# Performance work log

Measured on AMD Instinct MI355X. Metric: run time of the kernel, lower is better.

The kernel has to match this reference:

```python
import jax, jax.numpy as jnp
import numpy as np

TEMPERATURE = 8.0  # sqrt(d_k)
WINDOW = 2
GATE_THRESH = 0.5
NEG_INF = -1e30


def setup_inputs() -> dict:
    key = jax.random.key(0)
    k1, k2, k3, k4 = jax.random.split(key, 4)
    BH, L, D = 32, 2048, 64
    return {
        "q": jax.random.normal(k1, (BH, L, D), dtype=jnp.float32),
        "k": jax.random.normal(k2, (BH, L, D), dtype=jnp.float32),
        "v": jax.random.normal(k3, (BH, L, D), dtype=jnp.float32),
        "gate_w": jax.random.normal(k4, (1, D), dtype=jnp.float32) * 0.1,
        "gate_b": jnp.zeros((1,), dtype=jnp.float32),
    }


def reference(q, k, v, gate_w, gate_b):
    # q,k: [BH, L, D]; v: [BH, L, Dv]
    BH, Lq, D = q.shape
    Lk = k.shape[1]
    attn = jnp.einsum("bqd,bkd->bqk", q, k) / TEMPERATURE  # [BH, Lq, Lk]
    # per-query gate: if sigmoid(linear(q)) <= thresh, restrict to sliding window
    gate = jax.nn.sigmoid(jnp.einsum("bqd,od->bqo", q, gate_w) + gate_b) > GATE_THRESH  # [BH,Lq,1]
    i = jnp.arange(Lq)[:, None]
    j = jnp.arange(Lk)[None, :]
    window_ok = jnp.abs(i - j) <= WINDOW  # [Lq, Lk]; equals left=max(0,i-W), right=min(Lk,i+W+1)
    allowed = gate | window_ok[None, :, :]  # gate True -> full attention
    attn = jnp.where(allowed, attn, NEG_INF)
    attn = jax.nn.softmax(attn, axis=2)
    # dropout omitted (eval mode)
    out = jnp.einsum("bqk,bkd->bqd", attn, v)
    return out, attn
```

## Files before the change

kernel.cpp:

```cpp
#include <hip/hip_runtime.h>


typedef short bf16x8 __attribute__((ext_vector_type(8)));
typedef float f32x4  __attribute__((ext_vector_type(4)));

#define LSEQ 2048
#define DDIM 64
#define PB_STRIDE 36
#define OS_STRIDE 68

__device__ __forceinline__ unsigned short f2bf(float x) {
    unsigned int u = __float_as_uint(x);
    u += 0x7FFFu + ((u >> 16) & 1u);
    return (unsigned short)(u >> 16);
}

__device__ __forceinline__ unsigned int pk2f(float a, float b) {
    return (unsigned int)f2bf(a) | ((unsigned int)f2bf(b) << 16);
}

__device__ __forceinline__ unsigned int pk2u(unsigned short a, unsigned short b) {
    return (unsigned int)a | ((unsigned int)b << 16);
}

__device__ __forceinline__ float pick5(int jj, float e0, float e1, float e2,
                                       float e3, float e4) {
    float r = 0.f;
    r = (jj == 0) ? e0 : r;
    r = (jj == 1) ? e1 : r;
    r = (jj == 2) ? e2 : r;
    r = (jj == 3) ? e3 : r;
    r = (jj == 4) ? e4 : r;
    return r;
}

__global__ __launch_bounds__(256)
void dsa_prep(const float* __restrict__ K, const float* __restrict__ V,
              unsigned short* __restrict__ Kb, unsigned short* __restrict__ Vt)
{
    const int bh  = blockIdx.x >> 5;
    const int k0  = (blockIdx.x & 31) << 6;
    const int tid = threadIdx.x;
    __shared__ unsigned short tileT[64][73];

    const int key = tid >> 2;
    const int d0  = (tid & 3) << 4;
    const float* srcK = K + ((size_t)bh * LSEQ + k0 + key) * DDIM + d0;
    const float* srcV = V + ((size_t)bh * LSEQ + k0 + key) * DDIM + d0;
    {
        uint4 w0, w1;
        w0.x = pk2f(srcK[0],  srcK[1]);  w0.y = pk2f(srcK[2],  srcK[3]);
        w0.z = pk2f(srcK[4],  srcK[5]);  w0.w = pk2f(srcK[6],  srcK[7]);
        w1.x = pk2f(srcK[8],  srcK[9]);  w1.y = pk2f(srcK[10], srcK[11]);
        w1.z = pk2f(srcK[12], srcK[13]); w1.w = pk2f(srcK[14], srcK[15]);
        unsigned short* dst = Kb + ((size_t)bh * LSEQ + k0 + key) * DDIM + d0;
        *(uint4*)(dst)     = w0;
        *(uint4*)(dst + 8) = w1;
    }
    #pragma unroll
    for (int j = 0; j < 16; ++j) tileT[d0 + j][key] = f2bf(srcV[j]);
    __syncthreads();
    {
        const int d   = tid >> 2;
        const int kk0 = (tid & 3) << 4;
        uint4 w0, w1;
        w0.x = pk2u(tileT[d][kk0 + 0],  tileT[d][kk0 + 1]);
        w0.y = pk2u(tileT[d][kk0 + 2],  tileT[d][kk0 + 3]);
        w0.z = pk2u(tileT[d][kk0 + 4],  tileT[d][kk0 + 5]);
        w0.w = pk2u(tileT[d][kk0 + 6],  tileT[d][kk0 + 7]);
        w1.x = pk2u(tileT[d][kk0 + 8],  tileT[d][kk0 + 9]);
        w1.y = pk2u(tileT[d][kk0 + 10], tileT[d][kk0 + 11]);
        w1.z = pk2u(tileT[d][kk0 + 12], tileT[d][kk0 + 13]);
        w1.w = pk2u(tileT[d][kk0 + 14], tileT[d][kk0 + 15]);
        unsigned short* dst = Vt + (size_t)bh * DDIM * LSEQ + (size_t)d * LSEQ + k0 + kk0;
        *(uint4*)(dst)     = w0;
        *(uint4*)(dst + 8) = w1;
    }
}

__global__ __launch_bounds__(256)
void dsa_main(const float* __restrict__ Q,
              const unsigned short* __restrict__ Kb,
              const unsigned short* __restrict__ Vt,
              const float* __restrict__ K32,
              const float* __restrict__ V32,
              const float* __restrict__ GW,
              const float* __restrict__ GB,
              float* __restrict__ OUT,
              float* __restrict__ ATT)
{
    __shared__ float Pbuf[4][2][16 * PB_STRIDE];
    __shared__ float dsum[4][16];
    __shared__ float osum[4][16][OS_STRIDE];
    __shared__ int   sidx[64];
    __shared__ int   gShared;

    const int bx   = blockIdx.x;
    const int bh   = bx >> 5;
    const int q0   = (bx & 31) << 6;
    const int tid  = threadIdx.x;
    const int wave = tid >> 6;
    const int lane = tid & 63;
    const int m16  = lane & 15;
    const int quad = lane >> 4;

    const float* qb = Q + ((size_t)bh * LSEQ + q0) * DDIM;

    if (wave == 0) {
        const float* qr = qb + lane * DDIM;
        float a = 0.f;
        #pragma unroll 8
        for (int d = 0; d < DDIM; ++d) a += qr[d] * GW[d];
        a += GB[0];
        const bool gt = (a > 0.f);
        const unsigned long long b = __ballot(gt);
        const int below = __popcll(b & ((1ull << lane) - 1ull));
        const int gg    = __popcll(b);
        const int pos   = gt ? below : (gg + (lane - below));
        sidx[pos] = lane;
        if (lane == 0) gShared = gg;
    }
    __syncthreads();
    const int g = gShared;
    const int T = (g + 15) >> 4;

    const unsigned short* kbb = Kb + (size_t)bh * LSEQ * DDIM;
    const unsigned short* vtb = Vt + (size_t)bh * DDIM * LSEQ;
    const int kbase = wave << 9;

    for (int t = 0; t < T; ++t) {
        const int  myIdx = (t << 4) + m16;
        const bool valid = myIdx < g;
        const int  srow  = sidx[valid ? myIdx : (g - 1)];

        bf16x8 qfrag[2];
        {
            const float* qr = qb + srow * DDIM + (quad << 3);
            #pragma unroll
            for (int db = 0; db < 2; ++db) {
                const float* p = qr + db * 32;
                bf16x8 f;
                #pragma unroll
                for (int j = 0; j < 8; ++j) f[j] = (short)f2bf(p[j]);
                qfrag[db] = f;
            }
        }

        const unsigned short* kp0 = kbb + (size_t)(kbase + m16) * DDIM + (quad << 3);

        float lsum[4] = {0.f, 0.f, 0.f, 0.f};
        for (int kt = 0; kt < 16; ++kt) {
            const unsigned short* kp = kp0 + (size_t)(kt * 32) * DDIM;
            bf16x8 k0 = *(const bf16x8*)(kp);
            bf16x8 k1 = *(const bf16x8*)(kp + 32);
            bf16x8 k2 = *(const bf16x8*)(kp + 16 * DDIM);
            bf16x8 k3 = *(const bf16x8*)(kp + 16 * DDIM + 32);
            f32x4 a0 = {0.f, 0.f, 0.f, 0.f}, a1 = {0.f, 0.f, 0.f, 0.f};
            a0 = __builtin_amdgcn_mfma_f32_16x16x32_bf16(qfrag[0], k0, a0, 0, 0, 0);
            a0 = __builtin_amdgcn_mfma_f32_16x16x32_bf16(qfrag[1], k1, a0, 0, 0, 0);
            a1 = __builtin_amdgcn_mfma_f32_16x16x32_bf16(qfrag[0], k2, a1, 0, 0, 0);
            a1 = __builtin_amdgcn_mfma_f32_16x16x32_bf16(qfrag[1], k3, a1, 0, 0, 0);
            #pragma unroll
            for (int r = 0; r < 4; ++r)
                lsum[r] += __expf(a0[r] * 0.125f) + __expf(a1[r] * 0.125f);
        }
        #pragma unroll
        for (int r = 0; r < 4; ++r) {
            float x = lsum[r];
            x += __shfl_xor(x, 1); x += __shfl_xor(x, 2);
            x += __shfl_xor(x, 4); x += __shfl_xor(x, 8);
            if (m16 == 0) dsum[wave][(quad << 2) + r] = x;
        }
        __syncthreads();

        float inv[4];
        #pragma unroll
        for (int r = 0; r < 4; ++r) {
            const int rr = (quad << 2) + r;
            inv[r] = 1.0f / (dsum[0][rr] + dsum[1][rr] + dsum[2][rr] + dsum[3][rr]);
        }

        f32x4 oacc0 = {0.f,0.f,0.f,0.f}, oacc1 = {0.f,0.f,0.f,0.f};
        f32x4 oacc2 = {0.f,0.f,0.f,0.f}, oacc3 = {0.f,0.f,0.f,0.f};
        float* ap0 = ATT + ((size_t)(bh * LSEQ + q0 + srow)) * LSEQ + kbase + (quad << 3);
        const unsigned short* vp0 = vtb + (size_t)m16 * LSEQ + kbase + (quad << 3);

        #define COMPUTE(KT_) {                                                        \
            const unsigned short* kp = kp0 + (size_t)((KT_) * 32) * DDIM;             \
            bf16x8 k0 = *(const bf16x8*)(kp);                                         \
            bf16x8 k1 = *(const bf16x8*)(kp + 32);                                    \
            bf16x8 k2 = *(const bf16x8*)(kp + 16 * DDIM);                             \
            bf16x8 k3 = *(const bf16x8*)(kp + 16 * DDIM + 32);                        \
            f32x4 a0 = {0.f,0.f,0.f,0.f}, a1 = {0.f,0.f,0.f,0.f};                     \
            a0 = __builtin_amdgcn_mfma_f32_16x16x32_bf16(qfrag[0], k0, a0, 0, 0, 0);  \
            a0 = __builtin_amdgcn_mfma_f32_16x16x32_bf16(qfrag[1], k1, a0, 0, 0, 0);  \
            a1 = __builtin_amdgcn_mfma_f32_16x16x32_bf16(qfrag[0], k2, a1, 0, 0, 0);  \
            a1 = __builtin_amdgcn_mfma_f32_16x16x32_bf16(qfrag[1], k3, a1, 0, 0, 0);  \
            float* pw = &Pbuf[wave][(KT_) & 1][0];                                    \
            _Pragma("unroll")                                                         \
            for (int r = 0; r < 4; ++r) {                                             \
                const int prow = (quad << 2) + r;                                     \
                pw[prow * PB_STRIDE + m16]      = __expf(a0[r] * 0.125f) * inv[r];    \
                pw[prow * PB_STRIDE + 16 + m16] = __expf(a1[r] * 0.125f) * inv[r];    \
            }                                                                         \
        }

        #define CONSUME(KT_) {                                                        \
            const float* prd = &Pbuf[wave][(KT_) & 1][0] + m16 * PB_STRIDE + (quad << 3); \
            f32x4 p0 = *(const f32x4*)(prd);                                          \
            f32x4 p1 = *(const f32x4*)(prd + 4);                                      \
            const unsigned short* vp = vp0 + (KT_) * 32;                              \
            bf16x8 v0 = *(const bf16x8*)(vp);                                         \
            bf16x8 v1 = *(const bf16x8*)(vp + 16 * LSEQ);                             \
            bf16x8 v2 = *(const bf16x8*)(vp + 32 * LSEQ);                             \
            bf16x8 v3 = *(const bf16x8*)(vp + 48 * LSEQ);                             \
            if (valid) {                                                              \
                float* ap = ap0 + (KT_) * 32;                                         \
                *(f32x4*)(ap)     = p0;                                               \
                *(f32x4*)(ap + 4) = p1;                                               \
            }                                                                         \
            bf16x8 pf;                                                                \
            _Pragma("unroll")                                                         \
            for (int j = 0; j < 4; ++j) {                                             \
                pf[j]     = (short)f2bf(p0[j]);                                       \
                pf[4 + j] = (short)f2bf(p1[j]);                                       \
            }                                                                         \
            oacc0 = __builtin_amdgcn_mfma_f32_16x16x32_bf16(pf, v0, oacc0, 0, 0, 0);  \
            oacc1 = __builtin_amdgcn_mfma_f32_16x16x32_bf16(pf, v1, oacc1, 0, 0, 0);  \
            oacc2 = __builtin_amdgcn_mfma_f32_16x16x32_bf16(pf, v2, oacc2, 0, 0, 0);  \
            oacc3 = __builtin_amdgcn_mfma_f32_16x16x32_bf16(pf, v3, oacc3, 0, 0, 0);  \
        }

        COMPUTE(0)
        for (int kt = 1; kt < 16; ++kt) {
            CONSUME(kt - 1)
            COMPUTE(kt)
        }
        CONSUME(15)

        #undef COMPUTE
        #undef CONSUME

        #pragma unroll
        for (int r = 0; r < 4; ++r) {
            const int prow = (quad << 2) + r;
            osum[wave][prow][m16]      = oacc0[r];
            osum[wave][prow][16 + m16] = oacc1[r];
            osum[wave][prow][32 + m16] = oacc2[r];
            osum[wave][prow][48 + m16] = oacc3[r];
        }
        __syncthreads();

        #pragma unroll
        for (int rep = 0; rep < 4; ++rep) {
            const int idx = rep * 256 + tid;
            const int row = idx >> 6;
            const int col = idx & 63;
            const int gi  = (t << 4) + row;
            if (gi < g) {
                const float s = osum[0][row][col] + osum[1][row][col]
                              + osum[2][row][col] + osum[3][row][col];
                OUT[((size_t)(bh * LSEQ + q0 + sidx[gi])) * DDIM + col] = s;
            }
        }
        __syncthreads();
    }

    const int nw = 64 - g;
    for (int ii = wave; ii < nw; ii += 4) {
        const int row = sidx[g + ii];
        const int i   = q0 + row;
        const float qd = qb[row * DDIM + lane];

        float e[5];
        float denom = 0.f;
        #pragma unroll
        for (int jj = 0; jj < 5; ++jj) {
            const int  j  = i - 2 + jj;
            const bool ok = (j >= 0) && (j < LSEQ);
            const int  jc = ok ? j : 0;
            float tt = qd * K32[((size_t)bh * LSEQ + jc) * DDIM + lane];
            tt += __shfl_xor(tt, 1);  tt += __shfl_xor(tt, 2);
            tt += __shfl_xor(tt, 4);  tt += __shfl_xor(tt, 8);
            tt += __shfl_xor(tt, 16); tt += __shfl_xor(tt, 32);
            const float ee = ok ? __expf(tt * 0.125f) : 0.f;
            e[jj] = ee;
            denom += ee;
        }
        const float invd = 1.f / denom;
        #pragma unroll
        for (int jj = 0; jj < 5; ++jj) e[jj] *= invd;

        float o = 0.f;
        #pragma unroll
        for (int jj = 0; jj < 5; ++jj) {
            const int  j  = i - 2 + jj;
            const int  jc = (j >= 0 && j < LSEQ) ? j : 0;
            o += e[jj] * V32[((size_t)bh * LSEQ + jc) * DDIM + lane];
        }
        OUT[((size_t)(bh * LSEQ + i)) * DDIM + lane] = o;

        float* ar = ATT + ((size_t)(bh * LSEQ + i)) * LSEQ;
        const int jlo = i - 2;
        #pragma unroll
        for (int it = 0; it < 8; ++it) {
            const int c = (it << 8) + (lane << 2);
            f32x4 z = {0.f, 0.f, 0.f, 0.f};
            if (c + 3 >= jlo && c <= jlo + 4) {
                #pragma unroll
                for (int t4 = 0; t4 < 4; ++t4)
                    z[t4] = pick5(c + t4 - jlo, e[0], e[1], e[2], e[3], e[4]);
            }
            *(f32x4*)(ar + c) = z;
        }
    }
}

extern "C" void kernel_launch(void* const* d_in, const int* in_sizes, int n_in,
                              void* d_out, int out_size, void* d_ws, size_t ws_size,
                              hipStream_t stream) {
    const float* q  = (const float*)d_in[0];
    const float* k  = (const float*)d_in[1];
    const float* v  = (const float*)d_in[2];
    const float* gw = (const float*)d_in[3];
    const float* gb = (const float*)d_in[4];

    float* out  = (float*)d_out;
    float* attn = out + (size_t)32 * 2048 * 64;

    unsigned short* Kb = (unsigned short*)d_ws;
    unsigned short* Vt = Kb + (size_t)32 * 2048 * 64;

    dim3 block(256);
    dsa_prep<<<dim3(32 * 32), block, 0, stream>>>(k, v, Kb, Vt);
    dsa_main<<<dim3(32 * 32), block, 0, stream>>>(q, Kb, Vt, k, v, gw, gb, out, attn);
}
```

Baseline: 869.4 us.

## Halve query tile per block, swizzle block order, share LDS pool, nontemporal stores

Main kernel now processes 32 queries per block instead of 64, which doubles the grid to 2048 blocks. Block indices are remapped with an XCD-aware swizzle in both kernels. The P buffer and output-reduction scratch now share one LDS pool, so each block uses less LDS and more blocks can be resident. Attention and output writes become nontemporal stores to reduce cache pollution from the 512MB attention matrix, and two loops get partial unrolling. The cost is more per-block gate computation and less amortization of K/V reads across queries.

```diff
diff --git a/kernel.cpp b/kernel.cpp
--- a/kernel.cpp
+++ b/kernel.cpp
@@ -8,6 +8,7 @@
 #define DDIM 64
 #define PB_STRIDE 36
 #define OS_STRIDE 68
+#define POOLF 1168
 
 __device__ __forceinline__ unsigned short f2bf(float x) {
     unsigned int u = __float_as_uint(x);
@@ -38,8 +39,10 @@
 void dsa_prep(const float* __restrict__ K, const float* __restrict__ V,
               unsigned short* __restrict__ Kb, unsigned short* __restrict__ Vt)
 {
-    const int bh  = blockIdx.x >> 5;
-    const int k0  = (blockIdx.x & 31) << 6;
+    const int bx  = blockIdx.x;
+    const int w   = ((bx & 7) << 7) + (bx >> 3);
+    const int bh  = w >> 5;
+    const int k0  = (w & 31) << 6;
     const int tid = threadIdx.x;
     __shared__ unsigned short tileT[64][73];
 
@@ -89,15 +92,15 @@
               float* __restrict__ OUT,
               float* __restrict__ ATT)
 {
-    __shared__ float Pbuf[4][2][16 * PB_STRIDE];
+    __shared__ float Pool[4][POOLF];
     __shared__ float dsum[4][16];
-    __shared__ float osum[4][16][OS_STRIDE];
-    __shared__ int   sidx[64];
+    __shared__ int   sidx[32];
     __shared__ int   gShared;
 
     const int bx   = blockIdx.x;
-    const int bh   = bx >> 5;
-    const int q0   = (bx & 31) << 6;
+    const int w    = ((bx & 7) << 8) + (bx >> 3);
+    const int bh   = w >> 6;
+    const int q0   = (w & 63) << 5;
     const int tid  = threadIdx.x;
     const int wave = tid >> 6;
     const int lane = tid & 63;
@@ -107,17 +110,20 @@
     const float* qb = Q + ((size_t)bh * LSEQ + q0) * DDIM;
 
     if (wave == 0) {
-        const float* qr = qb + lane * DDIM;
+        const int row = lane & 31;
+        const float* qr = qb + row * DDIM;
         float a = 0.f;
         #pragma unroll 8
         for (int d = 0; d < DDIM; ++d) a += qr[d] * GW[d];
         a += GB[0];
-        const bool gt = (a > 0.f);
+        const bool gt = (lane < 32) && (a > 0.f);
         const unsigned long long b = __ballot(gt);
         const int below = __popcll(b & ((1ull << lane) - 1ull));
         const int gg    = __popcll(b);
-        const int pos   = gt ? below : (gg + (lane - below));
-        sidx[pos] = lane;
+        if (lane < 32) {
+            const int pos = gt ? below : (gg + (lane - below));
+            sidx[pos] = lane;
+        }
         if (lane == 0) gShared = gg;
     }
     __syncthreads();
@@ -149,6 +155,7 @@
         const unsigned short* kp0 = kbb + (size_t)(kbase + m16) * DDIM + (quad << 3);
 
         float lsum[4] = {0.f, 0.f, 0.f, 0.f};
+        #pragma unroll 2
         for (int kt = 0; kt < 16; ++kt) {
             const unsigned short* kp = kp0 + (size_t)(kt * 32) * DDIM;
             bf16x8 k0 = *(const bf16x8*)(kp);
@@ -196,7 +203,7 @@
             a0 = __builtin_amdgcn_mfma_f32_16x16x32_bf16(qfrag[1], k1, a0, 0, 0, 0);  \
             a1 = __builtin_amdgcn_mfma_f32_16x16x32_bf16(qfrag[0], k2, a1, 0, 0, 0);  \
             a1 = __builtin_amdgcn_mfma_f32_16x16x32_bf16(qfrag[1], k3, a1, 0, 0, 0);  \
-            float* pw = &Pbuf[wave][(KT_) & 1][0];                                    \
+            float* pw = &Pool[wave][((KT_) & 1) * 576];                               \
             _Pragma("unroll")                                                         \
             for (int r = 0; r < 4; ++r) {                                             \
                 const int prow = (quad << 2) + r;                                     \
@@ -206,7 +213,7 @@
         }
 
         #define CONSUME(KT_) {                                                        \
-            const float* prd = &Pbuf[wave][(KT_) & 1][0] + m16 * PB_STRIDE + (quad << 3); \
+            const float* prd = &Pool[wave][((KT_) & 1) * 576] + m16 * PB_STRIDE + (quad << 3); \
             f32x4 p0 = *(const f32x4*)(prd);                                          \
             f32x4 p1 = *(const f32x4*)(prd + 4);                                      \
             const unsigned short* vp = vp0 + (KT_) * 32;                              \
@@ -216,8 +223,8 @@
             bf16x8 v3 = *(const bf16x8*)(vp + 48 * LSEQ);                             \
             if (valid) {                                                              \
                 float* ap = ap0 + (KT_) * 32;                                         \
-                *(f32x4*)(ap)     = p0;                                               \
-                *(f32x4*)(ap + 4) = p1;                                               \
+                __builtin_nontemporal_store(p0, (f32x4*)(ap));                        \
+                __builtin_nontemporal_store(p1, (f32x4*)(ap + 4));                    \
             }                                                                         \
             bf16x8 pf;                                                                \
             _Pragma("unroll")                                                         \
@@ -232,6 +239,7 @@
         }
 
         COMPUTE(0)
+        #pragma unroll 2
         for (int kt = 1; kt < 16; ++kt) {
             CONSUME(kt - 1)
             COMPUTE(kt)
@@ -244,10 +252,11 @@
         #pragma unroll
         for (int r = 0; r < 4; ++r) {
             const int prow = (quad << 2) + r;
-            osum[wave][prow][m16]      = oacc0[r];
-            osum[wave][prow][16 + m16] = oacc1[r];
-            osum[wave][prow][32 + m16] = oacc2[r];
-            osum[wave][prow][48 + m16] = oacc3[r];
+            float* ow = &Pool[wave][prow * OS_STRIDE];
+            ow[m16]      = oacc0[r];
+            ow[16 + m16] = oacc1[r];
+            ow[32 + m16] = oacc2[r];
+            ow[48 + m16] = oacc3[r];
         }
         __syncthreads();
 
@@ -258,15 +267,18 @@
             const int col = idx & 63;
             const int gi  = (t << 4) + row;
             if (gi < g) {
-                const float s = osum[0][row][col] + osum[1][row][col]
-                              + osum[2][row][col] + osum[3][row][col];
-                OUT[((size_t)(bh * LSEQ + q0 + sidx[gi])) * DDIM + col] = s;
+                const float s = Pool[0][row * OS_STRIDE + col]
+                              + Pool[1][row * OS_STRIDE + col]
+                              + Pool[2][row * OS_STRIDE + col]
+                              + Pool[3][row * OS_STRIDE + col];
+                __builtin_nontemporal_store(
+                    s, &OUT[((size_t)(bh * LSEQ + q0 + sidx[gi])) * DDIM + col]);
             }
         }
         __syncthreads();
     }
 
-    const int nw = 64 - g;
+    const int nw = 32 - g;
     for (int ii = wave; ii < nw; ii += 4) {
         const int row = sidx[g + ii];
         const int i   = q0 + row;
@@ -298,7 +310,7 @@
             const int  jc = (j >= 0 && j < LSEQ) ? j : 0;
             o += e[jj] * V32[((size_t)bh * LSEQ + jc) * DDIM + lane];
         }
-        OUT[((size_t)(bh * LSEQ + i)) * DDIM + lane] = o;
+        __builtin_nontemporal_store(o, &OUT[((size_t)(bh * LSEQ + i)) * DDIM + lane]);
 
         float* ar = ATT + ((size_t)(bh * LSEQ + i)) * LSEQ;
         const int jlo = i - 2;
@@ -311,7 +323,7 @@
                 for (int t4 = 0; t4 < 4; ++t4)
                     z[t4] = pick5(c + t4 - jlo, e[0], e[1], e[2], e[3], e[4]);
             }
-            *(f32x4*)(ar + c) = z;
+            __builtin_nontemporal_store(z, (f32x4*)(ar + c));
         }
     }
 }
@@ -332,6 +344,6 @@
     unsigned short* Vt = Kb + (size_t)32 * 2048 * 64;
 
     dim3 block(256);
-    dsa_prep<<<dim3(32 * 32), block, 0, stream>>>(k, v, Kb, Vt);
-    dsa_main<<<dim3(32 * 32), block, 0, stream>>>(q, Kb, Vt, k, v, gw, gb, out, attn);
-}
+    dsa_prep<<<dim3(1024), block, 0, stream>>>(k, v, Kb, Vt);
+    dsa_main<<<dim3(2048), block, 0, stream>>>(q, Kb, Vt, k, v, gw, gb, out, attn);
+}
```

Result: slower. 957.5 us (+10.1%).
